# Kernel tuning notes

Measured on AMD Instinct MI355X. Metric: run time of the kernel, lower is better.

Reference implementation:

```python
import jax, jax.numpy as jnp
import numpy as np

N = 120000   # current nodes
F = 256      # num_feat
H = 256      # num_hidden
L = 64       # num_logits
E_MP = 1000000  # message-passing edges
E = 200000      # scored edges
PREV = [60000, 80000, 100000]
PROX_WEIGHT = 0.3


def setup_inputs() -> dict:
    key = jax.random.key(0)
    ks = jax.random.split(key, 40)
    n = lambda k, shape, s=0.05: jax.random.normal(k, shape, dtype=jnp.float32) * s
    inp = {}
    inp["x"] = n(ks[0], (N, F), 1.0)
    inp["mp_adj"] = jax.random.randint(ks[1], (2, E_MP), 0, N)
    inp["edges"] = jax.random.randint(ks[2], (2, E), 0, N)
    inp["index"] = jax.random.randint(ks[3], (E,), 0, E)
    inp["prev_emb0"] = n(ks[4], (PREV[0], H), 1.0)
    inp["prev_emb1"] = n(ks[5], (PREV[1], H), 1.0)
    inp["prev_emb2"] = n(ks[6], (PREV[2], H), 1.0)
    # Module_L params
    inp["gc1_W"] = n(ks[7], (F, H))
    inp["gc1_b"] = jnp.zeros((H,), jnp.float32)
    inp["gc2_W"] = n(ks[8], (H, H))
    inp["gc2_b"] = jnp.zeros((H,), jnp.float32)
    inp["linear_W"] = n(ks[9], (2 * H, H))
    inp["linear_b"] = jnp.zeros((H,), jnp.float32)
    inp["weight_lin"] = n(ks[10], (H, H))
    inp["bias_lin"] = jnp.zeros((H,), jnp.float32)
    inp["w_q"] = n(ks[11], (H, H))
    inp["w_k"] = n(ks[12], (H, H))
    inp["w_v"] = n(ks[13], (H, H))
    # ensemble params
    inp["ml_w1"] = n(ks[14], (2 * H, H)); inp["ml_b1"] = jnp.zeros((H,), jnp.float32)
    inp["ml_w2"] = n(ks[15], (H, 1));     inp["ml_b2"] = jnp.zeros((1,), jnp.float32)
    inp["ms_w1"] = n(ks[16], (2 * H, H)); inp["ms_b1"] = jnp.zeros((H,), jnp.float32)
    inp["ms_w2"] = n(ks[17], (H, 1));     inp["ms_b2"] = jnp.zeros((1,), jnp.float32)
    inp["msdr_w"] = n(ks[18], (L, H));    inp["msdr_b"] = jnp.zeros((H,), jnp.float32)
    # Module_S logits and precomputed score tables
    inp["logits"] = n(ks[19], (N, L), 1.0)
    inp["ms_train_score"] = jax.random.uniform(ks[20], (E,), dtype=jnp.float32)
    inp["prox_train_score"] = jax.random.uniform(ks[21], (E,), dtype=jnp.float32)
    return inp


def _gcn(x, W, b, src, dst, n_nodes):
    xw = x @ W
    loop = jnp.arange(n_nodes)
    s = jnp.concatenate([src, loop])
    d = jnp.concatenate([dst, loop])
    deg = jax.ops.segment_sum(jnp.ones_like(d, dtype=xw.dtype), d, num_segments=n_nodes)
    dinv = jax.lax.rsqrt(jnp.maximum(deg, 1.0))
    norm = (dinv[s] * dinv[d])[:, None]
    out = jax.ops.segment_sum(xw[s] * norm, d, num_segments=n_nodes)
    return out + b


def _mean_max(a, b):
    return jnp.concatenate([(a + b) * 0.5, jnp.maximum(a, b)], axis=1)


def reference(x, mp_adj, edges, index, prev_emb0, prev_emb1, prev_emb2,
              gc1_W, gc1_b, gc2_W, gc2_b, linear_W, linear_b,
              weight_lin, bias_lin, w_q, w_k, w_v,
              ml_w1, ml_b1, ml_w2, ml_b2, ms_w1, ms_b1, ms_w2, ms_b2,
              msdr_w, msdr_b, logits, ms_train_score, prox_train_score):
    src_mp, dst_mp = mp_adj[0], mp_adj[1]
    # --- Module_L: 2-layer GCN encoder (dropout = identity in eval) ---
    h = jnp.tanh(_gcn(x, gc1_W, gc1_b, src_mp, dst_mp, N))
    emb = jnp.tanh(_gcn(h, gc2_W, gc2_b, src_mp, dst_mp, N))

    # --- ragged per-window temporal attention over previous snapshots ---
    prev = [prev_emb0, prev_emb1, prev_emb2]
    T = len(prev)
    start = 0
    parts = []
    for i in range(T):
        end = prev[i].shape[0]
        if end == N:
            break
        # stack snapshots i..T-1 plus current, restricted to window [start:end)
        stack = jnp.stack([prev[j][start:end] for j in range(i, T)] + [emb[start:end]], axis=0)  # [S,n,H]
        q = emb[start:end] @ w_q              # [n,H]
        k = stack @ w_k                        # [S,n,H]
        v = stack @ w_v                        # [S,n,H]
        attn = jnp.einsum('nh,snh->ns', q, k) / np.sqrt(np.float32(H))
        w = jax.nn.softmax(attn, axis=-1)      # [n,S]
        parts.append(jnp.einsum('ns,snh->nh', w, v))
        start = end
    if start != N:
        parts.append(emb[start:] @ w_v)
    attn_emb = jnp.concatenate(parts, axis=0)  # [N,H]

    emb2 = jnp.tanh(jnp.concatenate([emb, attn_emb], axis=1) @ linear_W + linear_b)  # [N,H]

    # --- symmetric bilinear edge scores ---
    sym = (weight_lin + weight_lin.T) * 0.5
    es, ed = edges[0], edges[1]
    sim = ((emb2[es] @ sym) * emb2[ed] + bias_lin).sum(axis=1)
    ml_scores = jax.nn.sigmoid(sim)            # [E]

    # --- Module_S / Proximity: table lookups ---
    ms_scores = ms_train_score[index]
    prox_scores = prox_train_score[index]

    # --- ensemble weighted sum ---
    scores = jnp.stack([ml_scores, ms_scores, prox_scores], axis=1)  # [E,3]
    ml_feat = _mean_max(emb2[es], emb2[ed])                          # [E,2H]
    a_ml = jnp.tanh(jnp.tanh(ml_feat @ ml_w1 + ml_b1) @ ml_w2 + ml_b2)
    r0 = jnp.tanh(logits[es] @ msdr_w + msdr_b)
    r1 = jnp.tanh(logits[ed] @ msdr_w + msdr_b)
    a_ms = jnp.tanh(jnp.tanh(_mean_max(r0, r1) @ ms_w1 + ms_b1) @ ms_w2 + ms_b2)
    a_px = jnp.full_like(a_ml, PROX_WEIGHT)
    attn_w = jax.nn.softmax(jnp.concatenate([a_ml, a_ms, a_px], axis=1), axis=1)  # [E,3]
    final = jnp.clip((scores * attn_w).sum(axis=1), 0.0, 1.0)
    return final
```

## Files before the change

kernel.cpp:

```cpp
#include <hip/hip_runtime.h>
#include <hip/hip_bf16.h>

#define Nn_   120000
#define F_    256
#define H_    256
#define L_    64
#define EMP_  1000000
#define E_    200000
#define P0_   60000
#define P1_   80000
#define P2_   100000
#define PROXW 0.3f

typedef __attribute__((ext_vector_type(8))) short bf16x8;
typedef __attribute__((ext_vector_type(4))) float f32x4;

__device__ inline float bf2f(unsigned short u) {
    union { unsigned int i; float f; } x; x.i = ((unsigned int)u) << 16; return x.f;
}
__device__ inline unsigned short f2bf(float f) {
    union { float f; unsigned int i; } x; x.f = f;
    unsigned int r = x.i + 0x7fffu + ((x.i >> 16) & 1u);
    return (unsigned short)(r >> 16);
}
__device__ inline float tanh_fast(float x) {
    float e = __expf(2.0f * x);
    return 1.0f - 2.0f * __builtin_amdgcn_rcpf(e + 1.0f);
}
__device__ inline float sigmoid_fast(float z) {
    return __builtin_amdgcn_rcpf(1.0f + __expf(-z));
}
__device__ inline int lds_off(int row, int s) {
    return row * 64 + ((s ^ ((row >> 1) & 3)) << 4);
}
__device__ inline void gload_lds16(const void* g, void* l) {
    __builtin_amdgcn_global_load_lds((const __attribute__((address_space(1))) void*)g,
                                     (__attribute__((address_space(3))) void*)l, 16, 0, 0);
}
__device__ inline void unpk8(uint4 u, float* o) {
    o[0] = bf2f(u.x & 0xffff); o[1] = bf2f(u.x >> 16);
    o[2] = bf2f(u.y & 0xffff); o[3] = bf2f(u.y >> 16);
    o[4] = bf2f(u.z & 0xffff); o[5] = bf2f(u.z >> 16);
    o[6] = bf2f(u.w & 0xffff); o[7] = bf2f(u.w >> 16);
}

__global__ void k_count(const int* __restrict__ dst, int* __restrict__ cnt, int n) {
    int e = blockIdx.x * 256 + threadIdx.x;
    if (e < n) atomicAdd(&cnt[dst[e]], 1);
}
__global__ void k_block_reduce(const int* __restrict__ cnt, int* __restrict__ bsum, int n) {
    __shared__ int s[256];
    int i = blockIdx.x * 256 + threadIdx.x;
    s[threadIdx.x] = (i < n) ? cnt[i] : 0;
    __syncthreads();
    for (int o = 128; o > 0; o >>= 1) {
        if (threadIdx.x < o) s[threadIdx.x] += s[threadIdx.x + o];
        __syncthreads();
    }
    if (threadIdx.x == 0) bsum[blockIdx.x] = s[0];
}
__global__ void k_scan_bsum(int* bsum, int nb) {
    if (threadIdx.x == 0 && blockIdx.x == 0) {
        int acc = 0;
        for (int i = 0; i < nb; i++) { int v = bsum[i]; bsum[i] = acc; acc += v; }
    }
}
__global__ void k_scan_final(const int* __restrict__ cnt, const int* __restrict__ bsum,
                             int* __restrict__ rowp, int n, int etot) {
    __shared__ int s[256];
    int tid = threadIdx.x;
    int i = blockIdx.x * 256 + tid;
    int v = (i < n) ? cnt[i] : 0;
    s[tid] = v;
    __syncthreads();
    for (int o = 1; o < 256; o <<= 1) {
        int t = 0;
        if (tid >= o) t = s[tid - o];
        __syncthreads();
        s[tid] += t;
        __syncthreads();
    }
    if (i < n) rowp[i] = bsum[blockIdx.x] + s[tid] - v;
    if (i == 0 && blockIdx.x == 0) rowp[n] = etot;
}
__global__ void k_fill(const int* __restrict__ src, const int* __restrict__ dst,
                       const int* __restrict__ rowp, int* __restrict__ fill,
                       int* __restrict__ csr, int n) {
    int e = blockIdx.x * 256 + threadIdx.x;
    if (e < n) {
        int d = dst[e];
        int p = atomicAdd(&fill[d], 1);
        csr[rowp[d] + p] = src[e];
    }
}
__global__ void k_dinv(const int* __restrict__ cnt, float* __restrict__ dinv, int n) {
    int i = blockIdx.x * 256 + threadIdx.x;
    if (i < n) dinv[i] = rsqrtf((float)cnt[i] + 1.0f);
}

#define TM 64
#define TN 64
#define TK 16
template <bool TRANSB>
__global__ void gemm_tiled(const float* __restrict__ A, const float* __restrict__ B,
                           float* __restrict__ C, int M, int K, int N) {
    __shared__ float As[TK][TM + 4];
    __shared__ float Bs[TK][TN + 4];
    int tid = threadIdx.x;
    int tx = tid & 15, ty = tid >> 4;
    int row0 = blockIdx.y * TM, col0 = blockIdx.x * TN;
    int lr = tid >> 2, lc4 = (tid & 3) * 4;
    float acc[4][4] = {};
    for (int k0 = 0; k0 < K; k0 += TK) {
        {
            int gr = row0 + lr;
            float4 v = make_float4(0.f, 0.f, 0.f, 0.f);
            if (gr < M) v = *(const float4*)(A + (size_t)gr * K + k0 + lc4);
            As[lc4 + 0][lr] = v.x; As[lc4 + 1][lr] = v.y;
            As[lc4 + 2][lr] = v.z; As[lc4 + 3][lr] = v.w;
        }
        {
            int n = tid & 63, kk0 = tid >> 6;
#pragma unroll
            for (int p = 0; p < 4; p++) {
                int kk = kk0 + p * 4;
                if (TRANSB) Bs[kk][n] = B[(size_t)(col0 + n) * K + k0 + kk];
                else        Bs[kk][n] = B[(size_t)(k0 + kk) * N + col0 + n];
            }
        }
        __syncthreads();
#pragma unroll
        for (int kk = 0; kk < TK; kk++) {
            float4 a = *(const float4*)&As[kk][ty * 4];
            float4 b = *(const float4*)&Bs[kk][tx * 4];
            float av[4] = {a.x, a.y, a.z, a.w};
            float bv[4] = {b.x, b.y, b.z, b.w};
#pragma unroll
            for (int i = 0; i < 4; i++)
#pragma unroll
                for (int j = 0; j < 4; j++) acc[i][j] += av[i] * bv[j];
        }
        __syncthreads();
    }
#pragma unroll
    for (int i = 0; i < 4; i++) {
        int r = row0 + ty * 4 + i;
        if (r >= M) continue;
#pragma unroll
        for (int j = 0; j < 4; j++) C[(size_t)r * N + col0 + tx * 4 + j] = acc[i][j];
    }
}

__global__ void k_cvt(const float* __restrict__ in, unsigned short* __restrict__ out, int n4) {
    int i = blockIdx.x * 256 + threadIdx.x;
    if (i >= n4) return;
    float4 v = ((const float4*)in)[i];
    ushort4 o;
    o.x = f2bf(v.x); o.y = f2bf(v.y); o.z = f2bf(v.z); o.w = f2bf(v.w);
    ((ushort4*)out)[i] = o;
}
__global__ void k_transpose_cvt(const float* __restrict__ W, unsigned short* __restrict__ Wt,
                                int R, int C) {
    int c = blockIdx.x;
    for (int r = threadIdx.x; r < R; r += 256)
        Wt[(size_t)c * R + r] = f2bf(W[(size_t)r * C + c]);
}
__global__ void k_sym_cvt(const float* __restrict__ W, unsigned short* __restrict__ symb) {
    int r = blockIdx.x, c = threadIdx.x;
    symb[r * 256 + c] = f2bf(0.5f * (W[r * 256 + c] + W[c * 256 + r]));
}
__global__ void k_bt512(const float* __restrict__ linW, const float* __restrict__ W2w,
                        unsigned short* __restrict__ Bt) {
    int idx = blockIdx.x * 256 + threadIdx.x;
    int n = idx >> 9, k = idx & 511;
    float v = (k < 256) ? linW[(size_t)k * 256 + n] : W2w[(size_t)(k - 256) * 256 + n];
    Bt[idx] = f2bf(v);
}
__global__ void k_sumb(const float* __restrict__ b, float* __restrict__ out) {
    __shared__ float s[256];
    int tid = threadIdx.x;
    s[tid] = b[tid];
    __syncthreads();
    for (int o = 128; o > 0; o >>= 1) {
        if (tid < o) s[tid] += s[tid + o];
        __syncthreads();
    }
    if (tid == 0) out[0] = s[0];
}

__global__ __launch_bounds__(256)
void k_agg_bf(const unsigned short* __restrict__ xw, const int* __restrict__ rowp,
              const int* __restrict__ csr, const float* __restrict__ dinv,
              const float* __restrict__ bias, unsigned short* __restrict__ out) {
    int w = threadIdx.x >> 6, lane = threadIdx.x & 63;
    int v = blockIdx.x * 4 + w;
    if (v >= Nn_) return;
    const uint2* x64 = (const uint2*)xw;
    float a0 = 0.f, a1 = 0.f, a2 = 0.f, a3 = 0.f;
    int beg = rowp[v], end = rowp[v + 1];
    uint2 un = make_uint2(0, 0); float dn = 0.f;
    if (beg < end) {
        int s0 = csr[beg];
        dn = dinv[s0];
        un = x64[(size_t)s0 * 64 + lane];
    }
    for (int p = beg; p < end; ++p) {
        uint2 uc = un; float dc = dn;
        if (p + 1 < end) {
            int s1 = csr[p + 1];
            dn = dinv[s1];
            un = x64[(size_t)s1 * 64 + lane];
        }
        a0 += bf2f(uc.x & 0xffff) * dc;
        a1 += bf2f(uc.x >> 16) * dc;
        a2 += bf2f(uc.y & 0xffff) * dc;
        a3 += bf2f(uc.y >> 16) * dc;
    }
    float dv = dinv[v];
    uint2 us = x64[(size_t)v * 64 + lane];
    a0 = a0 * dv + bf2f(us.x & 0xffff) * dv * dv;
    a1 = a1 * dv + bf2f(us.x >> 16) * dv * dv;
    a2 = a2 * dv + bf2f(us.y & 0xffff) * dv * dv;
    a3 = a3 * dv + bf2f(us.y >> 16) * dv * dv;
    int c0 = lane * 4;
    float4 bv = *(const float4*)(bias + c0);
    uint2 ov;
    ov.x = (unsigned int)f2bf(tanh_fast(a0 + bv.x)) |
           ((unsigned int)f2bf(tanh_fast(a1 + bv.y)) << 16);
    ov.y = (unsigned int)f2bf(tanh_fast(a2 + bv.z)) |
           ((unsigned int)f2bf(tanh_fast(a3 + bv.w)) << 16);
    ((uint2*)out)[(size_t)v * 64 + lane] = ov;
}

template <bool BIAS, bool TANH>
__global__ __launch_bounds__(256)
void mfma_gemm(const unsigned short* __restrict__ A0, const unsigned short* __restrict__ A1,
               int Ksplit, int K, const unsigned short* __restrict__ Bt,
               const float* __restrict__ bias, unsigned short* __restrict__ Cb, int M) {
    __shared__ char lds[2][16384];
    int tid = threadIdx.x, lane = tid & 63, w = tid >> 6;
    int row0 = blockIdx.y * 128, col0 = blockIdx.x * 128;
    int wr = w >> 1, wc = w & 1;
    f32x4 acc[4][4] = {};
    int nk = K >> 5;

    auto stage = [&](int ks, int buf) {
        int k0 = ks << 5;
        #pragma unroll
        for (int j = 0; j < 4; ++j) {
            int ins = w + (j << 2);
            int lrow = ((ins & 7) << 4) + (lane >> 2);
            int p = lane & 3;
            int slog = p ^ ((lrow >> 1) & 3);
            char* ldst = lds[buf] + ((ins & 7) << 10) + ((ins >= 8) ? 8192 : 0);
            const unsigned short* src;
            if (ins < 8) {
                int grow = row0 + lrow;
                if (grow >= M) grow = M - 1;
                const unsigned short* Asrc; int kk, pitch;
                if (k0 < Ksplit) { Asrc = A0; kk = k0; pitch = Ksplit; }
                else             { Asrc = A1; kk = k0 - Ksplit; pitch = K - Ksplit; }
                src = Asrc + (size_t)grow * pitch + kk + (slog << 3);
            } else {
                int grow = col0 + lrow;
                src = Bt + (size_t)grow * K + k0 + (slog << 3);
            }
            gload_lds16(src, ldst);
        }
    };

    stage(0, 0);
    for (int ks = 0; ks < nk; ++ks) {
        int cur = ks & 1;
        if (ks + 1 < nk) {
            stage(ks + 1, cur ^ 1);
            asm volatile("s_waitcnt vmcnt(4)" ::: "memory");
        } else {
            asm volatile("s_waitcnt vmcnt(0)" ::: "memory");
        }
        __syncthreads();
        int s = lane >> 4, r16 = lane & 15;
        bf16x8 a[4], b[4];
        #pragma unroll
        for (int m = 0; m < 4; ++m) a[m] = *(const bf16x8*)(lds[cur] + lds_off(wr * 64 + m * 16 + r16, s));
        #pragma unroll
        for (int n = 0; n < 4; ++n) b[n] = *(const bf16x8*)(lds[cur] + 8192 + lds_off(wc * 64 + n * 16 + r16, s));
        #pragma unroll
        for (int m = 0; m < 4; ++m)
            #pragma unroll
            for (int n = 0; n < 4; ++n)
                acc[m][n] = __builtin_amdgcn_mfma_f32_16x16x32_bf16(a[m], b[n], acc[m][n], 0, 0, 0);
        __syncthreads();
    }
    int q = lane >> 4, r16 = lane & 15;
    float bv[4];
    #pragma unroll
    for (int n = 0; n < 4; ++n) bv[n] = BIAS ? bias[col0 + wc * 64 + n * 16 + r16] : 0.f;
    #pragma unroll
    for (int m = 0; m < 4; ++m) {
        #pragma unroll
        for (int i = 0; i < 4; ++i) {
            int row = row0 + wr * 64 + m * 16 + q * 4 + i;
            if (row >= M) continue;
            #pragma unroll
            for (int n = 0; n < 4; ++n) {
                int col = col0 + wc * 64 + n * 16 + r16;
                float v = acc[m][n][i];
                if (BIAS) v += bv[n];
                if (TANH) v = tanh_fast(v);
                Cb[(size_t)row * 256 + col] = f2bf(v);
            }
        }
    }
}

__global__ __launch_bounds__(256)
void k_attn_u2(const unsigned short* __restrict__ emb, const unsigned short* __restrict__ t,
               const float* __restrict__ p0, const float* __restrict__ p1,
               const float* __restrict__ p2, unsigned short* __restrict__ u) {
    int tid = threadIdx.x;
    int g = tid >> 4, l = tid & 15;
    int n = blockIdx.x * 16 + g;
    size_t eoff = (size_t)n * 256 + l * 16;
    const uint4* e16 = (const uint4*)(emb + eoff);
    uint4* u16 = (uint4*)(u + eoff);
    uint4 eb0 = e16[0], eb1 = e16[1];
    if (n >= P2_) { u16[0] = eb0; u16[1] = eb1; return; }
    float tv[16], ev[16];
    {
        const uint4* t16 = (const uint4*)(t + eoff);
        unpk8(t16[0], tv); unpk8(t16[1], tv + 8);
        unpk8(eb0, ev); unpk8(eb1, ev + 8);
    }
    float m = -3.0e38f, den = 0.f, o[16];
    #pragma unroll
    for (int i = 0; i < 16; i++) o[i] = 0.f;
    auto accum = [&](const float* sv) {
        float dt = 0.f;
        #pragma unroll
        for (int i = 0; i < 16; i++) dt += tv[i] * sv[i];
        dt += __shfl_xor(dt, 1);
        dt += __shfl_xor(dt, 2);
        dt += __shfl_xor(dt, 4);
        dt += __shfl_xor(dt, 8);
        float lg = dt * 0.0625f;
        float mn = fmaxf(m, lg);
        float s0 = __expf(m - mn), s1 = __expf(lg - mn);
        den = den * s0 + s1;
        #pragma unroll
        for (int i = 0; i < 16; i++) o[i] = o[i] * s0 + s1 * sv[i];
        m = mn;
    };
    auto accum_f32 = [&](const float* base) {
        float sv[16];
        const float4* b4 = (const float4*)(base + eoff);
        #pragma unroll
        for (int i = 0; i < 4; i++) {
            float4 q = b4[i];
            sv[4 * i] = q.x; sv[4 * i + 1] = q.y; sv[4 * i + 2] = q.z; sv[4 * i + 3] = q.w;
        }
        accum(sv);
    };
    if (n < P0_)      { accum_f32(p0); accum_f32(p1); accum_f32(p2); }
    else if (n < P1_) { accum_f32(p1); accum_f32(p2); }
    else              { accum_f32(p2); }
    accum(ev);
    float inv = __builtin_amdgcn_rcpf(den);
    unsigned short h[16];
    #pragma unroll
    for (int i = 0; i < 16; i++) h[i] = f2bf(o[i] * inv);
    uint4 r0, r1;
    r0.x = h[0] | ((unsigned int)h[1] << 16);  r0.y = h[2] | ((unsigned int)h[3] << 16);
    r0.z = h[4] | ((unsigned int)h[5] << 16);  r0.w = h[6] | ((unsigned int)h[7] << 16);
    r1.x = h[8] | ((unsigned int)h[9] << 16);  r1.y = h[10] | ((unsigned int)h[11] << 16);
    r1.z = h[12] | ((unsigned int)h[13] << 16); r1.w = h[14] | ((unsigned int)h[15] << 16);
    u16[0] = r0; u16[1] = r1;
}

template <bool SIM>
__global__ __launch_bounds__(256)
void mfma_edge(const unsigned short* __restrict__ srcemb, const unsigned short* __restrict__ gsrc,
               const int* __restrict__ es, const int* __restrict__ ed,
               const unsigned short* __restrict__ W1t, const float* __restrict__ b1,
               const float* __restrict__ w2, const float* __restrict__ sumb,
               float* __restrict__ a_pre, float* __restrict__ mlsc) {
    __shared__ char lds[8192 + 32768];
    __shared__ float red[64];
    int tid = threadIdx.x, lane = tid & 63, w = tid >> 6;
    int e0 = blockIdx.x * 64;
    int arow = tid >> 2, p = tid & 3;
    int ia = es[e0 + arow], ib = ed[e0 + arow];
    const unsigned short* ra = srcemb + (size_t)ia * 256;
    const unsigned short* rb = srcemb + (size_t)ib * 256;
    const unsigned short* rg = SIM ? (gsrc + (size_t)ia * 256) : nullptr;
    int slog = p ^ ((arow >> 1) & 3);
    if (tid < 64) red[tid] = 0.f;
    float simacc = 0.f;
    f32x4 acc[4][4] = {};
    int cbp = slog << 3;
    uint4 pa = *(const uint4*)(ra + cbp);
    uint4 pb = *(const uint4*)(rb + cbp);
    uint4 pg = make_uint4(0, 0, 0, 0);
    if (SIM) pg = *(const uint4*)(rg + cbp);
    for (int os = 0; os < 8; ++os) {
        __syncthreads();
        {
            float fa[8], fb[8];
            unpk8(pa, fa); unpk8(pb, fb);
            bf16x8 vm, vx;
            #pragma unroll
            for (int i = 0; i < 8; i++) {
                vm[i] = (short)f2bf(0.5f * (fa[i] + fb[i]));
                vx[i] = (short)f2bf(fmaxf(fa[i], fb[i]));
            }
            *(bf16x8*)(lds + arow * 64 + (p << 4)) = vm;
            *(bf16x8*)(lds + 4096 + arow * 64 + (p << 4)) = vx;
            if (SIM) {
                float fg[8];
                unpk8(pg, fg);
                #pragma unroll
                for (int i = 0; i < 8; i++) simacc += fg[i] * fb[i];
            }
        }
        #pragma unroll
        for (int j = 0; j < 8; ++j) {
            int ins = (j << 2) + w;
            int half = ins >> 4;
            int lrow = ((ins & 15) << 4) + (lane >> 2);
            int pp = lane & 3;
            int sl = pp ^ ((lrow >> 1) & 3);
            const unsigned short* src = W1t + (size_t)lrow * 512 + (half << 8) + (os << 5) + (sl << 3);
            gload_lds16(src, lds + 8192 + (ins << 10));
        }
        if (os < 7) {
            int cb = ((os + 1) << 5) + (slog << 3);
            pa = *(const uint4*)(ra + cb);
            pb = *(const uint4*)(rb + cb);
            if (SIM) pg = *(const uint4*)(rg + cb);
            if (SIM) asm volatile("s_waitcnt vmcnt(3)" ::: "memory");
            else     asm volatile("s_waitcnt vmcnt(2)" ::: "memory");
        } else {
            asm volatile("s_waitcnt vmcnt(0)" ::: "memory");
        }
        __syncthreads();
        int s = lane >> 4, r16 = lane & 15;
        #pragma unroll
        for (int half = 0; half < 2; ++half) {
            bf16x8 a[4], b[4];
            #pragma unroll
            for (int m2 = 0; m2 < 4; ++m2)
                a[m2] = *(const bf16x8*)(lds + half * 4096 + lds_off(m2 * 16 + r16, s));
            #pragma unroll
            for (int n2 = 0; n2 < 4; ++n2)
                b[n2] = *(const bf16x8*)(lds + 8192 + half * 16384 + lds_off(w * 64 + n2 * 16 + r16, s));
            #pragma unroll
            for (int m2 = 0; m2 < 4; ++m2)
                #pragma unroll
                for (int n2 = 0; n2 < 4; ++n2)
                    acc[m2][n2] = __builtin_amdgcn_mfma_f32_16x16x32_bf16(a[m2], b[n2], acc[m2][n2], 0, 0, 0);
        }
    }
    int q = lane >> 4, r16 = lane & 15;
    float b1c[4], w2c[4];
    #pragma unroll
    for (int n2 = 0; n2 < 4; ++n2) {
        int c = w * 64 + n2 * 16 + r16;
        b1c[n2] = b1[c]; w2c[n2] = w2[c];
    }
    #pragma unroll
    for (int m2 = 0; m2 < 4; ++m2) {
        #pragma unroll
        for (int i = 0; i < 4; ++i) {
            int row = m2 * 16 + q * 4 + i;
            float ps = 0.f;
            #pragma unroll
            for (int n2 = 0; n2 < 4; ++n2) ps += tanh_fast(acc[m2][n2][i] + b1c[n2]) * w2c[n2];
            ps += __shfl_xor(ps, 1);
            ps += __shfl_xor(ps, 2);
            ps += __shfl_xor(ps, 4);
            ps += __shfl_xor(ps, 8);
            if (r16 == 0) atomicAdd(&red[row], ps);
        }
    }
    if (SIM) {
        simacc += __shfl_xor(simacc, 1);
        simacc += __shfl_xor(simacc, 2);
        if (p == 0) mlsc[e0 + arow] = sigmoid_fast(simacc + sumb[0]);
    }
    __syncthreads();
    if (tid < 64) a_pre[e0 + tid] = red[tid];
}

__global__ void k_final(const float* __restrict__ apml, const float* __restrict__ apms,
                        const float* __restrict__ mlsc, const float* __restrict__ mstr,
                        const float* __restrict__ pxtr, const int* __restrict__ index,
                        const float* __restrict__ mlb2, const float* __restrict__ msb2,
                        float* __restrict__ out) {
    int e = blockIdx.x * 256 + threadIdx.x;
    if (e >= E_) return;
    float aml = tanh_fast(apml[e] + mlb2[0]);
    float ams = tanh_fast(apms[e] + msb2[0]);
    float apx = PROXW;
    float m = fmaxf(aml, fmaxf(ams, apx));
    float wml = __expf(aml - m), wms = __expf(ams - m), wpx = __expf(apx - m);
    float inv = __builtin_amdgcn_rcpf(wml + wms + wpx);
    int idx = index[e];
    float v = (mlsc[e] * wml + mstr[idx] * wms + pxtr[idx] * wpx) * inv;
    out[e] = fminf(fmaxf(v, 0.f), 1.f);
}

__global__ void k_sentinel(float* out, int n) {
    int i = blockIdx.x * 256 + threadIdx.x;
    if (i < n) out[i] = -12345.0f;
}

extern "C" void kernel_launch(void* const* d_in, const int* in_sizes, int n_in,
                              void* d_out, int out_size, void* d_ws, size_t ws_size,
                              hipStream_t stream) {
    const float* x     = (const float*)d_in[0];
    const int*   mp    = (const int*)d_in[1];
    const int*   edges = (const int*)d_in[2];
    const int*   index = (const int*)d_in[3];
    const float* p0    = (const float*)d_in[4];
    const float* p1    = (const float*)d_in[5];
    const float* p2    = (const float*)d_in[6];
    const float* gc1W  = (const float*)d_in[7];
    const float* gc1b  = (const float*)d_in[8];
    const float* gc2W  = (const float*)d_in[9];
    const float* gc2b  = (const float*)d_in[10];
    const float* linW  = (const float*)d_in[11];
    const float* linb  = (const float*)d_in[12];
    const float* wlin  = (const float*)d_in[13];
    const float* blin  = (const float*)d_in[14];
    const float* wq    = (const float*)d_in[15];
    const float* wk    = (const float*)d_in[16];
    const float* wv    = (const float*)d_in[17];
    const float* mlw1  = (const float*)d_in[18];
    const float* mlb1  = (const float*)d_in[19];
    const float* mlw2  = (const float*)d_in[20];
    const float* mlb2  = (const float*)d_in[21];
    const float* msw1  = (const float*)d_in[22];
    const float* msb1  = (const float*)d_in[23];
    const float* msw2  = (const float*)d_in[24];
    const float* msb2  = (const float*)d_in[25];
    const float* msdrW = (const float*)d_in[26];
    const float* msdrb = (const float*)d_in[27];
    const float* logits = (const float*)d_in[28];
    const float* mstr  = (const float*)d_in[29];
    const float* pxtr  = (const float*)d_in[30];
    float* out = (float*)d_out;

    const int* src_mp = mp;
    const int* dst_mp = mp + EMP_;
    const int* es = edges;
    const int* ed = edges + E_;

    char* ws = (char*)d_ws;
    size_t off = 0;
    auto alloc = [&](size_t bytes) -> char* {
        off = (off + 255) & ~(size_t)255;
        char* r = ws + off;
        off += bytes;
        return r;
    };
    const size_t NODE_BF = (size_t)Nn_ * 256 * 2;
    unsigned short* W0 = (unsigned short*)alloc(NODE_BF);
    unsigned short* W1 = (unsigned short*)alloc(NODE_BF);
    unsigned short* W2 = (unsigned short*)alloc(NODE_BF);
    unsigned short* W3 = (unsigned short*)alloc(NODE_BF);
    unsigned short* W4 = (unsigned short*)alloc(NODE_BF);
    unsigned short* W5 = (unsigned short*)alloc(NODE_BF);
    int*   cnt  = (int*)alloc((size_t)Nn_ * 4);
    int*   rowp = (int*)alloc((size_t)(Nn_ + 1) * 4);
    int*   fill = (int*)alloc((size_t)Nn_ * 4);
    int*   csr  = (int*)alloc((size_t)EMP_ * 4);
    float* dinv = (float*)alloc((size_t)Nn_ * 4);
    int*   bsum = (int*)alloc(512 * 4);
    float* Mqk  = (float*)alloc(65536 * 4);
    float* W2wf = (float*)alloc(65536 * 4);
    unsigned short* gc1Wt = (unsigned short*)alloc(65536 * 2);
    unsigned short* gc2Wt = (unsigned short*)alloc(65536 * 2);
    unsigned short* MqkT  = (unsigned short*)alloc(65536 * 2);
    unsigned short* Bt512 = (unsigned short*)alloc(131072 * 2);
    unsigned short* symb  = (unsigned short*)alloc(65536 * 2);
    unsigned short* msdrWt = (unsigned short*)alloc(16384 * 2);
    unsigned short* mlw1t = (unsigned short*)alloc(131072 * 2);
    unsigned short* msw1t = (unsigned short*)alloc(131072 * 2);
    float* apml = (float*)alloc((size_t)E_ * 4);
    float* apms = (float*)alloc((size_t)E_ * 4);
    float* mlsc = (float*)alloc((size_t)E_ * 4);
    float* sumb = (float*)alloc(256);

    if (off > ws_size) {
        k_sentinel<<<(E_ + 255) / 256, 256, 0, stream>>>(out, E_);
        return;
    }

    hipMemsetAsync(cnt, 0, (size_t)Nn_ * 4, stream);
    hipMemsetAsync(fill, 0, (size_t)Nn_ * 4, stream);

    const int NB = (Nn_ + 255) / 256;
    const int EB = (EMP_ + 255) / 256;

    k_cvt<<<30000, 256, 0, stream>>>(x, W0, Nn_ * 256 / 4);
    k_transpose_cvt<<<256, 256, 0, stream>>>(gc1W, gc1Wt, 256, 256);
    k_transpose_cvt<<<256, 256, 0, stream>>>(gc2W, gc2Wt, 256, 256);
    k_transpose_cvt<<<256, 256, 0, stream>>>(msdrW, msdrWt, 64, 256);
    k_transpose_cvt<<<256, 256, 0, stream>>>(mlw1, mlw1t, 512, 256);
    k_transpose_cvt<<<256, 256, 0, stream>>>(msw1, msw1t, 512, 256);
    k_sym_cvt<<<256, 256, 0, stream>>>(wlin, symb);
    k_sumb<<<1, 256, 0, stream>>>(blin, sumb);
    dim3 gSmall(4, 4);
    gemm_tiled<true><<<gSmall, 256, 0, stream>>>(wq, wk, Mqk, 256, 256, 256);
    gemm_tiled<false><<<gSmall, 256, 0, stream>>>(wv, linW + 256 * 256, W2wf, 256, 256, 256);
    k_transpose_cvt<<<256, 256, 0, stream>>>(Mqk, MqkT, 256, 256);
    k_bt512<<<512, 256, 0, stream>>>(linW, W2wf, Bt512);

    k_count<<<EB, 256, 0, stream>>>(dst_mp, cnt, EMP_);
    k_block_reduce<<<NB, 256, 0, stream>>>(cnt, bsum, Nn_);
    k_scan_bsum<<<1, 64, 0, stream>>>(bsum, NB);
    k_scan_final<<<NB, 256, 0, stream>>>(cnt, bsum, rowp, Nn_, EMP_);
    k_fill<<<EB, 256, 0, stream>>>(src_mp, dst_mp, rowp, fill, csr, EMP_);
    k_dinv<<<NB, 256, 0, stream>>>(cnt, dinv, Nn_);

    dim3 gFull(2, (Nn_ + 127) / 128);
    dim3 gT(2, (P2_ + 127) / 128);
    const int AGG_B = (Nn_ + 3) / 4;

    mfma_gemm<false, false><<<gFull, 256, 0, stream>>>(W0, W0, 256, 256, gc1Wt, nullptr, W1, Nn_);
    k_agg_bf<<<AGG_B, 256, 0, stream>>>(W1, rowp, csr, dinv, gc1b, W2);
    mfma_gemm<false, false><<<gFull, 256, 0, stream>>>(W2, W2, 256, 256, gc2Wt, nullptr, W1, Nn_);
    k_agg_bf<<<AGG_B, 256, 0, stream>>>(W1, rowp, csr, dinv, gc2b, W3);

    mfma_gemm<false, false><<<gT, 256, 0, stream>>>(W3, W3, 256, 256, MqkT, nullptr, W4, P2_);
    k_attn_u2<<<Nn_ / 16, 256, 0, stream>>>(W3, W4, p0, p1, p2, W4);

    mfma_gemm<true, true><<<gFull, 256, 0, stream>>>(W3, W4, 256, 512, Bt512, linb, W5, Nn_);

    mfma_gemm<false, false><<<gFull, 256, 0, stream>>>(W5, W5, 256, 256, symb, nullptr, W0, Nn_);

    k_cvt<<<7500, 256, 0, stream>>>(logits, W1, Nn_ * 64 / 4);
    mfma_gemm<true, true><<<gFull, 256, 0, stream>>>(W1, W1, 64, 64, msdrWt, msdrb, W2, Nn_);

    mfma_edge<true><<<E_ / 64, 256, 0, stream>>>(W5, W0, es, ed, mlw1t, mlb1, mlw2, sumb, apml, mlsc);
    mfma_edge<false><<<E_ / 64, 256, 0, stream>>>(W2, nullptr, es, ed, msw1t, msb1, msw2, sumb, apms, nullptr);

    k_final<<<(E_ + 255) / 256, 256, 0, stream>>>(apml, apms, mlsc, mstr, pxtr, index, mlb2, msb2, out);
}
```

Before: 1.050 ms.

## Double edge-kernel tile to 128 edges, prepack W1 for contiguous LDS loads

```diff
diff --git a/kernel.cpp b/kernel.cpp
--- a/kernel.cpp
+++ b/kernel.cpp
@@ -187,6 +187,18 @@
     }
     if (tid == 0) out[0] = s[0];
 }
+__global__ void k_packB(const float* __restrict__ Wsrc, unsigned short* __restrict__ P) {
+    int c = blockIdx.x * 256 + threadIdx.x;
+    if (c >= 16384) return;
+    int os = c >> 11, r = c & 2047;
+    int ins = r >> 6, lane = r & 63;
+    int n = ((ins & 15) << 4) + (lane >> 2);
+    int kb = ((ins >> 4) << 8) + (os << 5) + (((lane & 3) ^ ((n >> 1) & 3)) << 3);
+    bf16x8 v;
+#pragma unroll
+    for (int j = 0; j < 8; ++j) v[j] = (short)f2bf(Wsrc[(size_t)(kb + j) * 256 + n]);
+    *(bf16x8*)(P + (size_t)c * 8) = v;
+}
 
 __global__ __launch_bounds__(256)
 void k_agg_bf(const unsigned short* __restrict__ xw, const int* __restrict__ rowp,
@@ -278,19 +290,23 @@
         } else {
             asm volatile("s_waitcnt vmcnt(0)" ::: "memory");
         }
-        __syncthreads();
+        __builtin_amdgcn_s_barrier();
+        __builtin_amdgcn_sched_barrier(0);
         int s = lane >> 4, r16 = lane & 15;
         bf16x8 a[4], b[4];
         #pragma unroll
         for (int m = 0; m < 4; ++m) a[m] = *(const bf16x8*)(lds[cur] + lds_off(wr * 64 + m * 16 + r16, s));
         #pragma unroll
         for (int n = 0; n < 4; ++n) b[n] = *(const bf16x8*)(lds[cur] + 8192 + lds_off(wc * 64 + n * 16 + r16, s));
+        __builtin_amdgcn_s_setprio(1);
         #pragma unroll
         for (int m = 0; m < 4; ++m)
             #pragma unroll
             for (int n = 0; n < 4; ++n)
                 acc[m][n] = __builtin_amdgcn_mfma_f32_16x16x32_bf16(a[m], b[n], acc[m][n], 0, 0, 0);
-        __syncthreads();
+        __builtin_amdgcn_s_setprio(0);
+        __builtin_amdgcn_s_barrier();
+        __builtin_amdgcn_sched_barrier(0);
     }
     int q = lane >> 4, r16 = lane & 15;
     float bv[4];
@@ -378,32 +394,34 @@
 }
 
 template <bool SIM>
-__global__ __launch_bounds__(256)
-void mfma_edge(const unsigned short* __restrict__ srcemb, const unsigned short* __restrict__ gsrc,
-               const int* __restrict__ es, const int* __restrict__ ed,
-               const unsigned short* __restrict__ W1t, const float* __restrict__ b1,
-               const float* __restrict__ w2, const float* __restrict__ sumb,
-               float* __restrict__ a_pre, float* __restrict__ mlsc) {
-    __shared__ char lds[8192 + 32768];
-    __shared__ float red[64];
+__global__ __launch_bounds__(512, 4)
+void mfma_edge2(const unsigned short* __restrict__ srcemb, const unsigned short* __restrict__ gsrc,
+                const int* __restrict__ es, const int* __restrict__ ed,
+                const unsigned short* __restrict__ Pk, const float* __restrict__ b1,
+                const float* __restrict__ w2, const float* __restrict__ sumb,
+                float* __restrict__ a_pre, float* __restrict__ mlsc) {
+    __shared__ char lds[16384 + 32768];
+    __shared__ float red[128];
     int tid = threadIdx.x, lane = tid & 63, w = tid >> 6;
-    int e0 = blockIdx.x * 64;
+    int e0 = blockIdx.x * 128;
     int arow = tid >> 2, p = tid & 3;
-    int ia = es[e0 + arow], ib = ed[e0 + arow];
+    int erow = e0 + arow;
+    int ec = (erow < E_) ? erow : (E_ - 1);
+    int ia = es[ec], ib = ed[ec];
     const unsigned short* ra = srcemb + (size_t)ia * 256;
     const unsigned short* rb = srcemb + (size_t)ib * 256;
     const unsigned short* rg = SIM ? (gsrc + (size_t)ia * 256) : nullptr;
     int slog = p ^ ((arow >> 1) & 3);
-    if (tid < 64) red[tid] = 0.f;
+    int abase = ((arow >> 6) << 13) + ((arow & 63) << 6) + (p << 4);
+    if (tid < 128) red[tid] = 0.f;
     float simacc = 0.f;
     f32x4 acc[4][4] = {};
-    int cbp = slog << 3;
-    uint4 pa = *(const uint4*)(ra + cbp);
-    uint4 pb = *(const uint4*)(rb + cbp);
+    uint4 pa = *(const uint4*)(ra + (slog << 3));
+    uint4 pb = *(const uint4*)(rb + (slog << 3));
     uint4 pg = make_uint4(0, 0, 0, 0);
-    if (SIM) pg = *(const uint4*)(rg + cbp);
+    if (SIM) pg = *(const uint4*)(rg + (slog << 3));
+    #pragma unroll
     for (int os = 0; os < 8; ++os) {
-        __syncthreads();
         {
             float fa[8], fb[8];
             unpk8(pa, fa); unpk8(pb, fb);
@@ -413,8 +431,8 @@
                 vm[i] = (short)f2bf(0.5f * (fa[i] + fb[i]));
                 vx[i] = (short)f2bf(fmaxf(fa[i], fb[i]));
             }
-            *(bf16x8*)(lds + arow * 64 + (p << 4)) = vm;
-            *(bf16x8*)(lds + 4096 + arow * 64 + (p << 4)) = vx;
+            *(bf16x8*)(lds + abase) = vm;
+            *(bf16x8*)(lds + 4096 + abase) = vx;
             if (SIM) {
                 float fg[8];
                 unpk8(pg, fg);
@@ -423,55 +441,61 @@
             }
         }
         #pragma unroll
-        for (int j = 0; j < 8; ++j) {
-            int ins = (j << 2) + w;
-            int half = ins >> 4;
-            int lrow = ((ins & 15) << 4) + (lane >> 2);
-            int pp = lane & 3;
-            int sl = pp ^ ((lrow >> 1) & 3);
-            const unsigned short* src = W1t + (size_t)lrow * 512 + (half << 8) + (os << 5) + (sl << 3);
-            gload_lds16(src, lds + 8192 + (ins << 10));
+        for (int j = 0; j < 4; ++j) {
+            int ins = (j << 3) + w;
+            const unsigned short* src = Pk + ((os * 32 + ins) << 9) + (lane << 3);
+            gload_lds16(src, lds + 16384 + (ins << 10));
         }
         if (os < 7) {
             int cb = ((os + 1) << 5) + (slog << 3);
             pa = *(const uint4*)(ra + cb);
             pb = *(const uint4*)(rb + cb);
-            if (SIM) pg = *(const uint4*)(rg + cb);
-            if (SIM) asm volatile("s_waitcnt vmcnt(3)" ::: "memory");
-            else     asm volatile("s_waitcnt vmcnt(2)" ::: "memory");
+            if (SIM) {
+                pg = *(const uint4*)(rg + cb);
+                asm volatile("s_waitcnt vmcnt(3) lgkmcnt(0)" ::: "memory");
+            } else {
+                asm volatile("s_waitcnt vmcnt(2) lgkmcnt(0)" ::: "memory");
+            }
         } else {
-            asm volatile("s_waitcnt vmcnt(0)" ::: "memory");
-        }
-        __syncthreads();
+            asm volatile("s_waitcnt vmcnt(0) lgkmcnt(0)" ::: "memory");
+        }
+        __builtin_amdgcn_s_barrier();
+        __builtin_amdgcn_sched_barrier(0);
         int s = lane >> 4, r16 = lane & 15;
+        int ta = (w >> 2) << 13;
+        int qn = (w & 3) << 6;
         #pragma unroll
         for (int half = 0; half < 2; ++half) {
             bf16x8 a[4], b[4];
             #pragma unroll
             for (int m2 = 0; m2 < 4; ++m2)
-                a[m2] = *(const bf16x8*)(lds + half * 4096 + lds_off(m2 * 16 + r16, s));
+                a[m2] = *(const bf16x8*)(lds + ta + half * 4096 + lds_off(m2 * 16 + r16, s));
             #pragma unroll
             for (int n2 = 0; n2 < 4; ++n2)
-                b[n2] = *(const bf16x8*)(lds + 8192 + half * 16384 + lds_off(w * 64 + n2 * 16 + r16, s));
+                b[n2] = *(const bf16x8*)(lds + 16384 + half * 16384 + lds_off(qn + n2 * 16 + r16, s));
+            __builtin_amdgcn_s_setprio(1);
             #pragma unroll
             for (int m2 = 0; m2 < 4; ++m2)
                 #pragma unroll
                 for (int n2 = 0; n2 < 4; ++n2)
                     acc[m2][n2] = __builtin_amdgcn_mfma_f32_16x16x32_bf16(a[m2], b[n2], acc[m2][n2], 0, 0, 0);
-        }
+            __builtin_amdgcn_s_setprio(0);
+        }
+        __builtin_amdgcn_s_barrier();
+        __builtin_amdgcn_sched_barrier(0);
     }
     int q = lane >> 4, r16 = lane & 15;
     float b1c[4], w2c[4];
     #pragma unroll
     for (int n2 = 0; n2 < 4; ++n2) {
-        int c = w * 64 + n2 * 16 + r16;
+        int c = ((w & 3) << 6) + n2 * 16 + r16;
         b1c[n2] = b1[c]; w2c[n2] = w2[c];
     }
     #pragma unroll
     for (int m2 = 0; m2 < 4; ++m2) {
         #pragma unroll
         for (int i = 0; i < 4; ++i) {
-            int row = m2 * 16 + q * 4 + i;
+            int row = ((w >> 2) << 6) + m2 * 16 + q * 4 + i;
             float ps = 0.f;
             #pragma unroll
             for (int n2 = 0; n2 < 4; ++n2) ps += tanh_fast(acc[m2][n2][i] + b1c[n2]) * w2c[n2];
@@ -485,10 +509,10 @@
     if (SIM) {
         simacc += __shfl_xor(simacc, 1);
         simacc += __shfl_xor(simacc, 2);
-        if (p == 0) mlsc[e0 + arow] = sigmoid_fast(simacc + sumb[0]);
+        if (p == 0 && erow < E_) mlsc[erow] = sigmoid_fast(simacc + sumb[0]);
     }
     __syncthreads();
-    if (tid < 64) a_pre[e0 + tid] = red[tid];
+    if (tid < 128 && e0 + tid < E_) a_pre[e0 + tid] = red[tid];
 }
 
 __global__ void k_final(const float* __restrict__ apml, const float* __restrict__ apms,
@@ -584,8 +608,8 @@
     unsigned short* Bt512 = (unsigned short*)alloc(131072 * 2);
     unsigned short* symb  = (unsigned short*)alloc(65536 * 2);
     unsigned short* msdrWt = (unsigned short*)alloc(16384 * 2);
-    unsigned short* mlw1t = (unsigned short*)alloc(131072 * 2);
-    unsigned short* msw1t = (unsigned short*)alloc(131072 * 2);
+    unsigned short* mlPk  = (unsigned short*)alloc(131072 * 2);
+    unsigned short* msPk  = (unsigned short*)alloc(131072 * 2);
     float* apml = (float*)alloc((size_t)E_ * 4);
     float* apms = (float*)alloc((size_t)E_ * 4);
     float* mlsc = (float*)alloc((size_t)E_ * 4);
@@ -606,8 +630,8 @@
     k_transpose_cvt<<<256, 256, 0, stream>>>(gc1W, gc1Wt, 256, 256);
     k_transpose_cvt<<<256, 256, 0, stream>>>(gc2W, gc2Wt, 256, 256);
     k_transpose_cvt<<<256, 256, 0, stream>>>(msdrW, msdrWt, 64, 256);
-    k_transpose_cvt<<<256, 256, 0, stream>>>(mlw1, mlw1t, 512, 256);
-    k_transpose_cvt<<<256, 256, 0, stream>>>(msw1, msw1t, 512, 256);
+    k_packB<<<64, 256, 0, stream>>>(mlw1, mlPk);
+    k_packB<<<64, 256, 0, stream>>>(msw1, msPk);
     k_sym_cvt<<<256, 256, 0, stream>>>(wlin, symb);
     k_sumb<<<1, 256, 0, stream>>>(blin, sumb);
     dim3 gSmall(4, 4);
@@ -642,8 +666,9 @@
     k_cvt<<<7500, 256, 0, stream>>>(logits, W1, Nn_ * 64 / 4);
     mfma_gemm<true, true><<<gFull, 256, 0, stream>>>(W1, W1, 64, 64, msdrWt, msdrb, W2, Nn_);
 
-    mfma_edge<true><<<E_ / 64, 256, 0, stream>>>(W5, W0, es, ed, mlw1t, mlb1, mlw2, sumb, apml, mlsc);
-    mfma_edge<false><<<E_ / 64, 256, 0, stream>>>(W2, nullptr, es, ed, msw1t, msb1, msw2, sumb, apms, nullptr);
+    const int EB2 = (E_ + 127) / 128;
+    mfma_edge2<true><<<EB2, 512, 0, stream>>>(W5, W0, es, ed, mlPk, mlb1, mlw2, sumb, apml, mlsc);
+    mfma_edge2<false><<<EB2, 512, 0, stream>>>(W2, nullptr, es, ed, msPk, msb1, msw2, sumb, apms, nullptr);
 
     k_final<<<(E_ + 255) / 256, 256, 0, stream>>>(apml, apms, mlsc, mstr, pxtr, index, mlb2, msb2, out);
 }
```

Result: slower. 1.244 ms (+18.4%).
